# Kernel tuning notes

Hardware: AMD Instinct MI355X
Metric: run time of the kernel (lower is better)

## Reference

```python
import jax, jax.numpy as jnp
import numpy as np

N_QUBITS = 4
N_LAYERS = 3
N_OUTPUTS = 4
BATCH = 1048576


def _ry(t):
    # RY(t) = [[cos(t/2), -sin(t/2)], [sin(t/2), cos(t/2)]]; t may be scalar or (B,)
    c = jnp.cos(t / 2)
    s = jnp.sin(t / 2)
    m = jnp.stack([jnp.stack([c, -s], -1), jnp.stack([s, c], -1)], -2)
    return m.astype(jnp.complex64)


def _rx(t):
    c = jnp.cos(t / 2).astype(jnp.complex64)
    s = jnp.sin(t / 2).astype(jnp.complex64)
    return jnp.stack([jnp.stack([c, -1j * s], -1), jnp.stack([-1j * s, c], -1)], -2)


def _rz(t):
    e = jnp.exp(-1j * t.astype(jnp.complex64) / 2)  # exp(-i t/2)
    z = jnp.zeros_like(e)
    return jnp.stack([jnp.stack([e, z], -1), jnp.stack([z, jnp.conj(e)], -1)], -2)


def _apply_1q(state, U, q):
    # shared 2x2 gate U on wire q; state: (B, 2,2,2,2)
    s = jnp.moveaxis(state, q + 1, -1)
    s = jnp.einsum('ij,...j->...i', U, s)
    return jnp.moveaxis(s, -1, q + 1)


def _apply_1q_batched(state, U, q):
    # per-sample 2x2 gate U: (B,2,2) on wire q
    s = jnp.moveaxis(state, q + 1, -1)  # (B, ..., 2)
    s = jnp.einsum('bij,b...j->b...i', U, s)
    return jnp.moveaxis(s, -1, q + 1)


def _apply_cnot(state, c, t):
    s = jnp.moveaxis(state, (c + 1, t + 1), (-2, -1))  # (..., ctrl, tgt)
    s = jnp.stack([s[..., 0, :], s[..., 1, ::-1]], axis=-2)
    return jnp.moveaxis(s, (-2, -1), (c + 1, t + 1))


def setup_inputs() -> dict:
    key = jax.random.key(0)
    kx, kw = jax.random.split(key)
    x = jax.random.normal(kx, (BATCH, 2), dtype=jnp.float32)
    weights = jax.random.normal(kw, (N_LAYERS, N_QUBITS, 3), dtype=jnp.float32) * 0.1
    return {"x": x, "weights": weights}


def reference(x, weights):
    B = x.shape[0]
    # |0...0> state, batched
    state = jnp.zeros((B,) + (2,) * N_QUBITS, jnp.complex64)
    state = state.at[(slice(None),) + (0,) * N_QUBITS].set(1.0)
    # data encoding: RY(inputs[i % 2]) on wire i (per-sample angles)
    for i in range(N_QUBITS):
        state = _apply_1q_batched(state, _ry(x[:, i % 2]), i)
    # variational layers (shared angles)
    for l in range(N_LAYERS):
        for i in range(N_QUBITS):
            state = _apply_1q(state, _rx(weights[l, i, 0]), i)
            state = _apply_1q(state, _ry(weights[l, i, 1]), i)
            state = _apply_1q(state, _rz(weights[l, i, 2]), i)
        for i in range(N_QUBITS):
            state = _apply_cnot(state, i, (i + 1) % N_QUBITS)
    probs = state.real ** 2 + state.imag ** 2  # (B,2,2,2,2)
    outs = []
    for q in range(N_OUTPUTS):
        p = jnp.moveaxis(probs, q + 1, 1).reshape(B, 2, -1).sum(-1)
        outs.append(p[:, 0] - p[:, 1])  # <Z_q>
    return jnp.stack(outs, -1)  # (B, N_OUTPUTS)
```

## Files before the change

kernel.cpp:

```cpp
#include <hip/hip_runtime.h>
#include <hip/hip_bf16.h>


__global__ __launch_bounds__(256) void qnn_setup(const float* __restrict__ w,
                                                 float* __restrict__ C_out) {
    __shared__ float Ur[16][16];
    __shared__ float Ui[16][16];
    __shared__ float Csh[100];
    const int t = threadIdx.x;

    if (t < 100) Csh[t] = 0.0f;

    if (t < 16) {
        float ar[16], ai[16];
#pragma unroll
        for (int i = 0; i < 16; i++) { ar[i] = (i == t) ? 1.0f : 0.0f; ai[i] = 0.0f; }

#pragma unroll
        for (int l = 0; l < 3; l++) {
#pragma unroll
            for (int wq = 0; wq < 4; wq++) {
                const int st = 1 << (3 - wq);
                float th, s, c;
                th = w[(l * 4 + wq) * 3 + 0] * 0.5f;
                s = __sinf(th); c = __cosf(th);
#pragma unroll
                for (int lo = 0; lo < 16; lo++) if (!(lo & st)) {
                    const int hi = lo | st;
                    const float arl = ar[lo], ail = ai[lo], arh = ar[hi], aih = ai[hi];
                    ar[lo] = c * arl + s * aih;
                    ai[lo] = c * ail - s * arh;
                    ar[hi] = c * arh + s * ail;
                    ai[hi] = c * aih - s * arl;
                }
                th = w[(l * 4 + wq) * 3 + 1] * 0.5f;
                s = __sinf(th); c = __cosf(th);
#pragma unroll
                for (int lo = 0; lo < 16; lo++) if (!(lo & st)) {
                    const int hi = lo | st;
                    const float arl = ar[lo], ail = ai[lo], arh = ar[hi], aih = ai[hi];
                    ar[lo] = c * arl - s * arh;
                    ai[lo] = c * ail - s * aih;
                    ar[hi] = s * arl + c * arh;
                    ai[hi] = s * ail + c * aih;
                }
                th = w[(l * 4 + wq) * 3 + 2] * 0.5f;
                s = __sinf(th); c = __cosf(th);
#pragma unroll
                for (int lo = 0; lo < 16; lo++) if (!(lo & st)) {
                    const int hi = lo | st;
                    const float arl = ar[lo], ail = ai[lo], arh = ar[hi], aih = ai[hi];
                    ar[lo] = c * arl + s * ail;
                    ai[lo] = c * ail - s * arl;
                    ar[hi] = c * arh - s * aih;
                    ai[hi] = c * aih + s * arh;
                }
            }
#pragma unroll
            for (int ci = 0; ci < 4; ci++) {
                const int cst = 1 << (3 - ci);
                const int tst = 1 << (3 - ((ci + 1) & 3));
#pragma unroll
                for (int k = 0; k < 16; k++) if ((k & cst) && !(k & tst)) {
                    const int k2 = k | tst;
                    const float tr = ar[k], ti = ai[k];
                    ar[k] = ar[k2]; ai[k] = ai[k2];
                    ar[k2] = tr;    ai[k2] = ti;
                }
            }
        }
#pragma unroll
        for (int i = 0; i < 16; i++) { Ur[i][t] = ar[i]; Ui[i][t] = ai[i]; }
    }
    __syncthreads();

    {
        const int i = t >> 4;
        const int j = t & 15;
        float m0 = 0.f, m1 = 0.f, m2 = 0.f, m3 = 0.f;
#pragma unroll
        for (int k = 0; k < 16; k++) {
            const float r = Ur[k][i] * Ur[k][j] + Ui[k][i] * Ui[k][j];
            m0 += ((k >> 3) & 1) ? -r : r;
            m1 += ((k >> 2) & 1) ? -r : r;
            m2 += ((k >> 1) & 1) ? -r : r;
            m3 += ((k >> 0) & 1) ? -r : r;
        }
        const int mm = ((i >> 3) & 1) + ((i >> 1) & 1) + ((j >> 3) & 1) + ((j >> 1) & 1);
        const int nn = ((i >> 2) & 1) + (i & 1) + ((j >> 2) & 1) + (j & 1);
        const int mn4 = (mm * 5 + nn) * 4;
        atomicAdd(&Csh[mn4 + 0], m0);
        atomicAdd(&Csh[mn4 + 1], m1);
        atomicAdd(&Csh[mn4 + 2], m2);
        atomicAdd(&Csh[mn4 + 3], m3);
    }
    __syncthreads();
    if (t < 100) C_out[t] = Csh[t];
}


__device__ __forceinline__ float2 mul2(float2 a, float2 b) {
    return make_float2(a.x * b.x, a.y * b.y);
}
__device__ __forceinline__ float2 fma2(float s, float2 a, float2 b) {
    return make_float2(fmaf(s, a.x, b.x), fmaf(s, a.y, b.y));
}

__global__ __launch_bounds__(256) void qnn_batch(const float2* __restrict__ x2,
                                                 const float4* __restrict__ C4,
                                                 float4* __restrict__ out,
                                                 int B) {
    const int t = threadIdx.x;
    const int bs = blockIdx.x * 1024;

    float4 cv[25];
#pragma unroll
    for (int i = 0; i < 25; i++) cv[i] = C4[i];

    if (bs + 1024 <= B) {
        const int sA0 = bs + t;
        const float2 xA0 = x2[sA0];
        const float2 xB0 = x2[sA0 + 256];
        const float2 xA1 = x2[sA0 + 512];
        const float2 xB1 = x2[sA0 + 768];
        __builtin_amdgcn_sched_barrier(0);

#pragma unroll
        for (int k = 0; k < 2; k++) {
            const float2 xA = k ? xA1 : xA0;
            const float2 xB = k ? xB1 : xB0;
            const float2 s0 = make_float2(__sinf(xA.x * 0.5f), __sinf(xB.x * 0.5f));
            const float2 c0 = make_float2(__cosf(xA.x * 0.5f), __cosf(xB.x * 0.5f));
            const float2 s1 = make_float2(__sinf(xA.y * 0.5f), __sinf(xB.y * 0.5f));
            const float2 c1 = make_float2(__cosf(xA.y * 0.5f), __cosf(xB.y * 0.5f));

            const float2 cc0 = mul2(c0, c0), ss0 = mul2(s0, s0), cs0 = mul2(c0, s0);
            const float2 cc1 = mul2(c1, c1), ss1 = mul2(s1, s1), cs1 = mul2(c1, s1);
            const float2 p0[5] = { mul2(cc0, cc0), mul2(cc0, cs0), mul2(cs0, cs0),
                                   mul2(cs0, ss0), mul2(ss0, ss0) };
            const float2 p1[5] = { mul2(cc1, cc1), mul2(cc1, cs1), mul2(cs1, cs1),
                                   mul2(cs1, ss1), mul2(ss1, ss1) };

            float2 a0 = make_float2(0.f, 0.f), a1 = a0, a2 = a0, a3 = a0;
#pragma unroll
            for (int m = 0; m < 5; m++)
#pragma unroll
                for (int n = 0; n < 5; n++) {
                    const float4 cvv = cv[m * 5 + n];
                    const float2 pp = mul2(p0[m], p1[n]);
                    a0 = fma2(cvv.x, pp, a0);
                    a1 = fma2(cvv.y, pp, a1);
                    a2 = fma2(cvv.z, pp, a2);
                    a3 = fma2(cvv.w, pp, a3);
                }
            const int sA = bs + k * 512 + t;
            out[sA]       = make_float4(a0.x, a1.x, a2.x, a3.x);
            out[sA + 256] = make_float4(a0.y, a1.y, a2.y, a3.y);
        }
    } else {
#pragma unroll
        for (int k = 0; k < 4; k++) {
            const int s = bs + k * 256 + t;
            if (s < B) {
                const float2 xv = x2[s];
                const float st0 = __sinf(xv.x * 0.5f), ct0 = __cosf(xv.x * 0.5f);
                const float st1 = __sinf(xv.y * 0.5f), ct1 = __cosf(xv.y * 0.5f);
                const float cc0 = ct0 * ct0, ss0 = st0 * st0, cs0 = ct0 * st0;
                const float cc1 = ct1 * ct1, ss1 = st1 * st1, cs1 = ct1 * st1;
                const float q0[5] = { cc0 * cc0, cc0 * cs0, cs0 * cs0, cs0 * ss0, ss0 * ss0 };
                const float q1[5] = { cc1 * cc1, cc1 * cs1, cs1 * cs1, cs1 * ss1, ss1 * ss1 };
                float o0 = 0.f, o1 = 0.f, o2 = 0.f, o3 = 0.f;
#pragma unroll
                for (int m = 0; m < 5; m++)
#pragma unroll
                    for (int n = 0; n < 5; n++) {
                        const float4 cvv = cv[m * 5 + n];
                        const float pp = q0[m] * q1[n];
                        o0 = fmaf(cvv.x, pp, o0);
                        o1 = fmaf(cvv.y, pp, o1);
                        o2 = fmaf(cvv.z, pp, o2);
                        o3 = fmaf(cvv.w, pp, o3);
                    }
                out[s] = make_float4(o0, o1, o2, o3);
            }
        }
    }
}

extern "C" void kernel_launch(void* const* d_in, const int* in_sizes, int n_in,
                              void* d_out, int out_size, void* d_ws, size_t ws_size,
                              hipStream_t stream) {
    const float* x = (const float*)d_in[0];
    const float* w = (const float*)d_in[1];
    float* C = (float*)d_ws;
    const int B = in_sizes[0] / 2;

    qnn_setup<<<1, 256, 0, stream>>>(w, C);

    int grid = (B + 1023) / 1024;
    if (grid < 1) grid = 1;
    qnn_batch<<<grid, 256, 0, stream>>>((const float2*)x, (const float4*)C,
                                        (float4*)d_out, B);
}
```

Baseline: 76.84 us.

## Fuse setup into batch kernel, recomputing coefficient table per block

Merges the single-block setup kernel into the batch kernel, so every block recomputes the 16x16 circuit unitary and the 100-entry coefficient table in shared memory instead of reading it from a workspace written by a prior launch. The gate sin/cos values are precomputed in parallel into shared memory, and the sched_barrier after the x loads is removed. This drops one kernel launch and its serial dependency. In exchange each of about 1024 blocks repeats the setup work, which mostly runs on 16 threads and adds a few barriers before the batch work can start.

```diff
diff --git a/kernel.cpp b/kernel.cpp
--- a/kernel.cpp
+++ b/kernel.cpp
@@ -2,14 +2,31 @@
 #include <hip/hip_bf16.h>
 
 
-__global__ __launch_bounds__(256) void qnn_setup(const float* __restrict__ w,
-                                                 float* __restrict__ C_out) {
+__device__ __forceinline__ float2 mul2(float2 a, float2 b) {
+    return make_float2(a.x * b.x, a.y * b.y);
+}
+__device__ __forceinline__ float2 fma2(float s, float2 a, float2 b) {
+    return make_float2(fmaf(s, a.x, b.x), fmaf(s, a.y, b.y));
+}
+
+__global__ __launch_bounds__(256) void qnn_fused(const float2* __restrict__ x2,
+                                                 const float* __restrict__ w,
+                                                 float4* __restrict__ out,
+                                                 int B) {
     __shared__ float Ur[16][16];
     __shared__ float Ui[16][16];
-    __shared__ float Csh[100];
+    __shared__ float gs[36];
+    __shared__ float gc[36];
+    __shared__ __align__(16) float Csh[100];
     const int t = threadIdx.x;
 
     if (t < 100) Csh[t] = 0.0f;
+    if (t < 36) {
+        const float th = w[t] * 0.5f;
+        gs[t] = __sinf(th);
+        gc[t] = __cosf(th);
+    }
+    __syncthreads();
 
     if (t < 16) {
         float ar[16], ai[16];
@@ -21,39 +38,36 @@
 #pragma unroll
             for (int wq = 0; wq < 4; wq++) {
                 const int st = 1 << (3 - wq);
-                float th, s, c;
-                th = w[(l * 4 + wq) * 3 + 0] * 0.5f;
-                s = __sinf(th); c = __cosf(th);
+                const int g0 = (l * 4 + wq) * 3;
+                const float sx = gs[g0 + 0], cx = gc[g0 + 0];
+                const float sy = gs[g0 + 1], cy = gc[g0 + 1];
+                const float sz = gs[g0 + 2], cz = gc[g0 + 2];
 #pragma unroll
                 for (int lo = 0; lo < 16; lo++) if (!(lo & st)) {
                     const int hi = lo | st;
                     const float arl = ar[lo], ail = ai[lo], arh = ar[hi], aih = ai[hi];
-                    ar[lo] = c * arl + s * aih;
-                    ai[lo] = c * ail - s * arh;
-                    ar[hi] = c * arh + s * ail;
-                    ai[hi] = c * aih - s * arl;
+                    ar[lo] = cx * arl + sx * aih;
+                    ai[lo] = cx * ail - sx * arh;
+                    ar[hi] = cx * arh + sx * ail;
+                    ai[hi] = cx * aih - sx * arl;
                 }
-                th = w[(l * 4 + wq) * 3 + 1] * 0.5f;
-                s = __sinf(th); c = __cosf(th);
 #pragma unroll
                 for (int lo = 0; lo < 16; lo++) if (!(lo & st)) {
                     const int hi = lo | st;
                     const float arl = ar[lo], ail = ai[lo], arh = ar[hi], aih = ai[hi];
-                    ar[lo] = c * arl - s * arh;
-                    ai[lo] = c * ail - s * aih;
-                    ar[hi] = s * arl + c * arh;
-                    ai[hi] = s * ail + c * aih;
+                    ar[lo] = cy * arl - sy * arh;
+                    ai[lo] = cy * ail - sy * aih;
+                    ar[hi] = sy * arl + cy * arh;
+                    ai[hi] = sy * ail + cy * aih;
                 }
-                th = w[(l * 4 + wq) * 3 + 2] * 0.5f;
-                s = __sinf(th); c = __cosf(th);
 #pragma unroll
                 for (int lo = 0; lo < 16; lo++) if (!(lo & st)) {
                     const int hi = lo | st;
                     const float arl = ar[lo], ail = ai[lo], arh = ar[hi], aih = ai[hi];
-                    ar[lo] = c * arl + s * ail;
-                    ai[lo] = c * ail - s * arl;
-                    ar[hi] = c * arh - s * aih;
-                    ai[hi] = c * aih + s * arh;
+                    ar[lo] = cz * arl + sz * ail;
+                    ai[lo] = cz * ail - sz * arl;
+                    ar[hi] = cz * arh - sz * aih;
+                    ai[hi] = cz * aih + sz * arh;
                 }
             }
 #pragma unroll
@@ -95,27 +109,13 @@
         atomicAdd(&Csh[mn4 + 3], m3);
     }
     __syncthreads();
-    if (t < 100) C_out[t] = Csh[t];
-}
 
-
-__device__ __forceinline__ float2 mul2(float2 a, float2 b) {
-    return make_float2(a.x * b.x, a.y * b.y);
-}
-__device__ __forceinline__ float2 fma2(float s, float2 a, float2 b) {
-    return make_float2(fmaf(s, a.x, b.x), fmaf(s, a.y, b.y));
-}
-
-__global__ __launch_bounds__(256) void qnn_batch(const float2* __restrict__ x2,
-                                                 const float4* __restrict__ C4,
-                                                 float4* __restrict__ out,
-                                                 int B) {
-    const int t = threadIdx.x;
-    const int bs = blockIdx.x * 1024;
-
+    const float4* __restrict__ Csh4 = (const float4*)Csh;
     float4 cv[25];
 #pragma unroll
-    for (int i = 0; i < 25; i++) cv[i] = C4[i];
+    for (int i = 0; i < 25; i++) cv[i] = Csh4[i];
+
+    const int bs = blockIdx.x * 1024;
 
     if (bs + 1024 <= B) {
         const int sA0 = bs + t;
@@ -123,7 +123,6 @@
         const float2 xB0 = x2[sA0 + 256];
         const float2 xA1 = x2[sA0 + 512];
         const float2 xB1 = x2[sA0 + 768];
-        __builtin_amdgcn_sched_barrier(0);
 
 #pragma unroll
         for (int k = 0; k < 2; k++) {
@@ -192,13 +191,9 @@
                               hipStream_t stream) {
     const float* x = (const float*)d_in[0];
     const float* w = (const float*)d_in[1];
-    float* C = (float*)d_ws;
     const int B = in_sizes[0] / 2;
-
-    qnn_setup<<<1, 256, 0, stream>>>(w, C);
 
     int grid = (B + 1023) / 1024;
     if (grid < 1) grid = 1;
-    qnn_batch<<<grid, 256, 0, stream>>>((const float2*)x, (const float4*)C,
-                                        (float4*)d_out, B);
+    qnn_fused<<<grid, 256, 0, stream>>>((const float2*)x, w, (float4*)d_out, B);
 }
```

Measured after the change: 79.20 us. +3.1%, slower.
